# Kernel tuning notes

Measured on AMD Instinct MI355X. Metric: run time of the kernel, lower is better.

Reference implementation:

```python
import jax, jax.numpy as jnp
import numpy as np

N_HEADS = 16
EPS = 1e-12  # F.normalize default eps


def setup_inputs() -> dict:
    key = jax.random.key(0)
    ks = jax.random.split(key, 12)
    bs, qlen, dim = 2, 2048, 2048
    s = 0.02
    return {
        "input": jax.random.normal(ks[0], (bs, qlen, dim), jnp.float32),
        "mask": jax.random.randint(ks[1], (bs, qlen), 0, 2, jnp.int64),
        "Wq": jax.random.normal(ks[2], (dim, dim), jnp.float32) * s,
        "bq": jax.random.normal(ks[3], (dim,), jnp.float32) * s,
        "Wk": jax.random.normal(ks[4], (dim, dim), jnp.float32) * s,
        "bk": jax.random.normal(ks[5], (dim,), jnp.float32) * s,
        "Wv": jax.random.normal(ks[6], (dim, dim), jnp.float32) * s,
        "bv": jax.random.normal(ks[7], (dim,), jnp.float32) * s,
        "Wo": jax.random.normal(ks[8], (dim, dim), jnp.float32) * s,
        "bo": jax.random.normal(ks[9], (dim,), jnp.float32) * s,
        "attention_scale": jnp.asarray(1.0 / np.sqrt(dim // N_HEADS), jnp.float32),
    }


def _l2norm(x):
    n = jnp.sqrt(jnp.sum(x * x, axis=-1, keepdims=True))
    return x / jnp.maximum(n, EPS)


def reference(input, mask, Wq, bq, Wk, bk, Wv, bv, Wo, bo, attention_scale):
    bs, qlen, dim = input.shape
    dph = dim // N_HEADS

    def shape(x):  # [b, s, dim] -> [b, h, s, dph]
        return x.reshape(bs, -1, N_HEADS, dph).transpose(0, 2, 1, 3)

    q = shape(input @ Wq.T + bq)
    k = shape(input @ Wk.T + bk)
    v = shape(input @ Wv.T + bv)

    # normalized (cosine) attention with learned scale
    q = _l2norm(q) * attention_scale
    k = _l2norm(k)

    scores = jnp.einsum("bhqd,bhkd->bhqk", q, k)
    masked = (mask == 0)[:, None, None, :]  # [b,1,1,klen]
    scores = jnp.where(masked, -jnp.inf, scores)
    weights = jax.nn.softmax(scores.astype(jnp.float32), axis=-1).astype(scores.dtype)
    # dropout p=0.0 / eval mode -> identity
    context = jnp.einsum("bhqk,bhkd->bhqd", weights, v)
    context = context.transpose(0, 2, 1, 3).reshape(bs, qlen, dim)
    return context @ Wo.T + bo
```

## Files before the change

kernel.cpp:

```cpp
#include <hip/hip_runtime.h>
#include <hip/hip_bf16.h>
#include <stdint.h>


typedef __attribute__((ext_vector_type(8))) short bf16x8;
typedef __attribute__((ext_vector_type(4))) float f32x4;
typedef __attribute__((ext_vector_type(8))) unsigned short u16x8;

#define XN 8388608L
#define WN 4194304L

__device__ __forceinline__ float bf2f(unsigned short u) {
  union { unsigned int i; float f; } v; v.i = ((unsigned int)u) << 16; return v.f;
}
__device__ __forceinline__ unsigned short f2bf(float f) {
  union { float f; unsigned int i; } u; u.f = f;
  unsigned int r = u.i + 0x7FFFu + ((u.i >> 16) & 1u);
  return (unsigned short)(r >> 16);
}

__device__ __forceinline__ void gload_lds16(const void* g, void* l) {
  __builtin_amdgcn_global_load_lds((__attribute__((address_space(1))) void*)g,
                                   (__attribute__((address_space(3))) void*)l,
                                   16, 0, 0);
}

__global__ __launch_bounds__(256) void cast5_kernel(
    const float* __restrict__ x,  const float* __restrict__ w0,
    const float* __restrict__ w1, const float* __restrict__ w2,
    const float* __restrict__ w3, unsigned short* __restrict__ dst,
    const int* __restrict__ mask, float* __restrict__ biasf)
{
  const long total8 = (XN + 4 * WN) >> 3;
  const long tid0 = (long)blockIdx.x * blockDim.x + threadIdx.x;
  const long stride = (long)gridDim.x * blockDim.x;
  for (long i = tid0; i < total8; i += stride) {
    long e = i << 3;
    const float* src; long off;
    if (e < XN) { src = x; off = e; }
    else {
      long r = e - XN;
      int wi = (int)(r >> 22);
      off = r & (WN - 1);
      src = (wi == 0) ? w0 : (wi == 1) ? w1 : (wi == 2) ? w2 : w3;
    }
    const float4* p = (const float4*)(src + off);
    float4 a = p[0], b = p[1];
    u16x8 o;
    o[0] = f2bf(a.x); o[1] = f2bf(a.y); o[2] = f2bf(a.z); o[3] = f2bf(a.w);
    o[4] = f2bf(b.x); o[5] = f2bf(b.y); o[6] = f2bf(b.z); o[7] = f2bf(b.w);
    *(u16x8*)(dst + e) = o;
  }
  for (long j = tid0; j < 4096; j += stride)
    biasf[j] = (mask[j] != 0) ? 0.f : -1.0e5f;
}

template<int MODE>
__global__ __launch_bounds__(256) void gemm2(
    const unsigned short* __restrict__ A, const unsigned short* __restrict__ Bmat,
    const float* __restrict__ bias0, const float* __restrict__ bias1,
    void* __restrict__ Cout)
{
  constexpr int NWG = (MODE == 0) ? 1024 : 512;
  __shared__ unsigned short As[2][4096];
  __shared__ unsigned short Bs[2][4096];

  const int bid = blockIdx.x;
  const int id = (bid & 7) * (NWG / 8) + (bid >> 3);

  int mat, bx, by;
  if (MODE == 0)      { mat = id >> 9; int rem = id & 511; bx = rem & 15; by = rem >> 4; }
  else if (MODE == 1) { mat = 0; bx = id & 31; by = id >> 5; }
  else                { mat = 0; bx = id & 15; by = id >> 4; }

  const unsigned short* Bb = (MODE == 0) ? (Bmat + (long)mat * WN) : Bmat;
  const float* bias = (MODE == 0) ? (mat ? bias1 : bias0) : bias0;

  const int t    = threadIdx.x;
  const int lane = t & 63;
  const int w    = t >> 6;
  const int wr   = w >> 1, wc = w & 1;
  const int l15  = lane & 15;
  const int koff = (lane >> 4) * 8;
  const int lg4  = (lane >> 4) * 4;

  const unsigned short* Ag0 = A  + (long)(by * 128 + (t >> 2)) * 2048 + (t & 3) * 8;
  const unsigned short* Bg0 = Bb + (long)(bx * 128 + (t >> 2)) * 2048 + (t & 3) * 8;

  f32x4 acc[4][4];
  const f32x4 zero = {0.f, 0.f, 0.f, 0.f};
  #pragma unroll
  for (int m = 0; m < 4; m++)
    #pragma unroll
    for (int n = 0; n < 4; n++) acc[m][n] = zero;

  auto stage = [&](int buf, int kk) {
    const long ko = (long)kk * 32;
    gload_lds16(Ag0 + ko,              &As[buf][t * 8]);
    gload_lds16(Ag0 + 64 * 2048 + ko,  &As[buf][t * 8 + 2048]);
    gload_lds16(Bg0 + ko,              &Bs[buf][t * 8]);
    gload_lds16(Bg0 + 64 * 2048 + ko,  &Bs[buf][t * 8 + 2048]);
  };

  auto body = [&](int bufR, int kk, int bufW) {
    if (kk + 1 < 64) stage(bufW, kk + 1);
    bf16x8 af[4], bfr[4];
    #pragma unroll
    for (int m = 0; m < 4; m++)
      af[m] = *(const bf16x8*)&As[bufR][(wr * 64 + m * 16 + l15) * 32 + koff];
    #pragma unroll
    for (int n = 0; n < 4; n++)
      bfr[n] = *(const bf16x8*)&Bs[bufR][(wc * 64 + n * 16 + l15) * 32 + koff];
    __builtin_amdgcn_s_setprio(1);
    #pragma unroll
    for (int m = 0; m < 4; m++)
      #pragma unroll
      for (int n = 0; n < 4; n++)
        acc[m][n] = __builtin_amdgcn_mfma_f32_16x16x32_bf16(af[m], bfr[n], acc[m][n], 0, 0, 0);
    __builtin_amdgcn_s_setprio(0);
    asm volatile("s_waitcnt vmcnt(0)" ::: "memory");
    __builtin_amdgcn_s_barrier();
    __builtin_amdgcn_sched_barrier(0);
  };

  stage(0, 0);
  asm volatile("s_waitcnt vmcnt(0)" ::: "memory");
  __builtin_amdgcn_s_barrier();
  __builtin_amdgcn_sched_barrier(0);

  for (int kk = 0; kk < 64; kk += 2) {
    body(0, kk,     1);
    body(1, kk + 1, 0);
  }

  #pragma unroll
  for (int m = 0; m < 4; m++) {
    const int row = by * 128 + wr * 64 + m * 16 + lg4;
    #pragma unroll
    for (int n = 0; n < 4; n++) {
      const int col = bx * 128 + wc * 64 + n * 16 + l15;
      #pragma unroll
      for (int r = 0; r < 4; r++) {
        float v = acc[m][n][r];
        if (MODE == 0) {
          v += bias[col];
          ((unsigned short*)Cout + (long)mat * XN)[(long)(row + r) * 2048 + col] = f2bf(v);
        } else if (MODE == 1) {
          v += bias[row + r];
          ((unsigned short*)Cout)[(long)(row + r) * 2048 + (col & 2047)
                                  + (long)(col >> 11) * 4194304] = f2bf(v);
        } else {
          v += bias[col];
          ((float*)Cout)[(long)(row + r) * 2048 + col] = v;
        }
      }
    }
  }
}

__global__ __launch_bounds__(256) void norm_qk(unsigned short* __restrict__ Q,
                                               unsigned short* __restrict__ Kb,
                                               const float* __restrict__ scale_p)
{
  const int w = threadIdx.x >> 6, lane = threadIdx.x & 63;
  const long id = (long)blockIdx.x * 4 + w;
  const int isK = id >= 65536;
  const long p = isK ? id - 65536 : id;
  unsigned short* base = (isK ? Kb : Q) + (p >> 4) * 2048 + (p & 15) * 128 + lane * 2;
  unsigned int v = *(const unsigned int*)base;
  float x0 = bf2f((unsigned short)(v & 0xffffu));
  float x1 = bf2f((unsigned short)(v >> 16));
  float ss = x0 * x0 + x1 * x1;
  ss += __shfl_xor(ss, 1);  ss += __shfl_xor(ss, 2);  ss += __shfl_xor(ss, 4);
  ss += __shfl_xor(ss, 8);  ss += __shfl_xor(ss, 16); ss += __shfl_xor(ss, 32);
  float inv = rsqrtf(fmaxf(ss, 1e-24f));
  if (!isK) inv *= *scale_p;
  unsigned int o = (unsigned int)f2bf(x0 * inv) | ((unsigned int)f2bf(x1 * inv) << 16);
  *(unsigned int*)base = o;
}

__global__ __launch_bounds__(256, 2) void attn_kernel(
    const unsigned short* __restrict__ Q,
    const unsigned short* __restrict__ Kg_,
    const unsigned short* __restrict__ Vt_,
    const float* __restrict__ biasArr,
    unsigned short* __restrict__ ctx)
{
  __shared__ unsigned char KS[16384];
  __shared__ unsigned char VS[16384];
  __shared__ unsigned short Pl[4][32][72];

  const int bh = blockIdx.y, b = bh >> 4, h = bh & 15;
  const int t = threadIdx.x, w = t >> 6, lane = t & 63;
  const int l15 = lane & 15, lg = lane >> 4;
  const int xork = (l15 & 7) << 4;
  const int qrow0 = blockIdx.x * 128 + w * 32;

  bf16x8 aq[2][4];
  #pragma unroll
  for (int m = 0; m < 2; m++)
    #pragma unroll
    for (int dk = 0; dk < 4; dk++)
      aq[m][dk] = *(const bf16x8*)&Q[(long)(b * 2048 + qrow0 + m * 16 + l15) * 2048
                                     + h * 128 + dk * 32 + lg * 8];

  const char* Kgp = (const char*)(Kg_ + (long)b * 2048 * 2048 + h * 128);
  const char* Vgp = (const char*)(Vt_ + (long)bh * 128 * 2048);
  const int rK = t >> 4;
  const int rV = t >> 3;
  const char* srcK0 = Kgp + (long)rK * 4096 + (((t & 15) * 16) ^ ((rK & 7) << 4));
  const char* srcV0 = Vgp + (long)rV * 4096 + (((t & 7) * 16) ^ ((rV & 7) << 4));
  char* dstK0 = (char*)KS + t * 16;
  char* dstV0 = (char*)VS + t * 16;

  f32x4 o[2][8]; float den[2][4];
  const f32x4 zero = {0.f, 0.f, 0.f, 0.f};
  #pragma unroll
  for (int m = 0; m < 2; m++) {
    #pragma unroll
    for (int df = 0; df < 8; df++) o[m][df] = zero;
    #pragma unroll
    for (int r = 0; r < 4; r++) den[m][r] = 0.f;
  }

  const char* KSc = (const char*)KS;
  const char* VSc = (const char*)VS;
  int cK[4], cV2[2];
  #pragma unroll
  for (int dk = 0; dk < 4; dk++) cK[dk] = (dk * 64 + lg * 16) ^ xork;
  #pragma unroll
  for (int kk = 0; kk < 2; kk++) cV2[kk] = (kk * 64 + lg * 16) ^ xork;
  const int rowK = l15 * 256, rowV = l15 * 128;

  #pragma unroll
  for (int i = 0; i < 4; i++) gload_lds16(srcK0 + i * 65536,  dstK0 + i * 4096);
  #pragma unroll
  for (int i = 0; i < 4; i++) gload_lds16(srcV0 + i * 131072, dstV0 + i * 4096);

  const float* brow = biasArr + b * 2048 + l15;
  const float L2E = 1.44269504088896f;

  for (int kt = 0; kt < 32; kt++) {
    const int k0 = kt * 64;
    asm volatile("s_waitcnt vmcnt(4)" ::: "memory");
    __builtin_amdgcn_s_barrier();
    __builtin_amdgcn_sched_barrier(0);

    float bn[4];
    #pragma unroll
    for (int n = 0; n < 4; n++) bn[n] = brow[k0 + n * 16];

    f32x4 s[2][4];
    #pragma unroll
    for (int m = 0; m < 2; m++)
      #pragma unroll
      for (int n = 0; n < 4; n++) s[m][n] = zero;
    __builtin_amdgcn_s_setprio(1);
    #pragma unroll
    for (int n = 0; n < 4; n++) {
      #pragma unroll
      for (int dk = 0; dk < 4; dk++) {
        bf16x8 bk = *(const bf16x8*)(KSc + n * 4096 + rowK + cK[dk]);
        s[0][n] = __builtin_amdgcn_mfma_f32_16x16x32_bf16(aq[0][dk], bk, s[0][n], 0, 0, 0);
        s[1][n] = __builtin_amdgcn_mfma_f32_16x16x32_bf16(aq[1][dk], bk, s[1][n], 0, 0, 0);
      }
    }
    __builtin_amdgcn_s_setprio(0);

    #pragma unroll
    for (int n = 0; n < 4; n++) {
      #pragma unroll
      for (int m = 0; m < 2; m++) {
        #pragma unroll
        for (int r = 0; r < 4; r++) {
          float e = exp2f(fmaf(s[m][n][r], L2E, bn[n]));
          den[m][r] += e;
          Pl[w][m * 16 + lg * 4 + r][n * 16 + l15] = f2bf(e);
        }
      }
    }

    asm volatile("s_waitcnt vmcnt(0)" ::: "memory");
    __builtin_amdgcn_s_barrier();
    __builtin_amdgcn_sched_barrier(0);
    if (kt < 31) {
      const long kof = (long)(kt + 1) * 262144;
      #pragma unroll
      for (int i = 0; i < 4; i++) gload_lds16(srcK0 + kof + i * 65536, dstK0 + i * 4096);
    }

    #pragma unroll
    for (int kk = 0; kk < 2; kk++) {
      bf16x8 ap0 = *(const bf16x8*)&Pl[w][l15][kk * 32 + lg * 8];
      bf16x8 ap1 = *(const bf16x8*)&Pl[w][16 + l15][kk * 32 + lg * 8];
      bf16x8 bv[8];
      #pragma unroll
      for (int df = 0; df < 8; df++)
        bv[df] = *(const bf16x8*)(VSc + df * 2048 + rowV + cV2[kk]);
      __builtin_amdgcn_s_setprio(1);
      #pragma unroll
      for (int df = 0; df < 8; df++) {
        o[0][df] = __builtin_amdgcn_mfma_f32_16x16x32_bf16(ap0, bv[df], o[0][df], 0, 0, 0);
        o[1][df] = __builtin_amdgcn_mfma_f32_16x16x32_bf16(ap1, bv[df], o[1][df], 0, 0, 0);
      }
      __builtin_amdgcn_s_setprio(0);
    }

    __builtin_amdgcn_s_barrier();
    __builtin_amdgcn_sched_barrier(0);
    if (kt < 31) {
      const long vof = (long)(kt + 1) * 128;
      #pragma unroll
      for (int i = 0; i < 4; i++) gload_lds16(srcV0 + vof + i * 131072, dstV0 + i * 4096);
    }
  }

  #pragma unroll
  for (int m = 0; m < 2; m++)
    #pragma unroll
    for (int r = 0; r < 4; r++) {
      float d = den[m][r];
      d += __shfl_xor(d, 1); d += __shfl_xor(d, 2);
      d += __shfl_xor(d, 4); d += __shfl_xor(d, 8);
      den[m][r] = 1.0f / d;
    }
  #pragma unroll
  for (int m = 0; m < 2; m++) {
    const long row = b * 2048 + qrow0 + m * 16 + lg * 4;
    #pragma unroll
    for (int df = 0; df < 8; df++) {
      const int col = h * 128 + df * 16 + l15;
      #pragma unroll
      for (int r = 0; r < 4; r++)
        ctx[(row + r) * 2048 + col] = f2bf(o[m][df][r] * den[m][r]);
    }
  }
}

extern "C" void kernel_launch(void* const* d_in, const int* in_sizes, int n_in,
                              void* d_out, int out_size, void* d_ws, size_t ws_size,
                              hipStream_t stream) {
  const float* x    = (const float*)d_in[0];
  const int*   mask = (const int*)d_in[1];
  const float* Wq   = (const float*)d_in[2];
  const float* bq   = (const float*)d_in[3];
  const float* Wk   = (const float*)d_in[4];
  const float* bk   = (const float*)d_in[5];
  const float* Wv   = (const float*)d_in[6];
  const float* bv   = (const float*)d_in[7];
  const float* Wo   = (const float*)d_in[8];
  const float* bo   = (const float*)d_in[9];
  const float* asc  = (const float*)d_in[10];
  float* out = (float*)d_out;

  unsigned short* w   = (unsigned short*)d_ws;
  unsigned short* Xb  = w;
  unsigned short* Wqb = Xb  + XN;
  unsigned short* Wvb = Wqb + 2 * WN;
  unsigned short* Wob = Wvb + WN;
  unsigned short* Qb  = Wob + WN;
  unsigned short* Kbf = Qb  + XN;
  unsigned short* Vt  = Kbf + XN;
  float*          Bias = (float*)(Vt + XN);
  unsigned short* Ctx = Xb;

  cast5_kernel<<<2048, 256, 0, stream>>>(x, Wq, Wk, Wv, Wo, Xb, mask, Bias);

  gemm2<0><<<1024, 256, 0, stream>>>(Xb, Wqb, bq, bk, Qb);
  gemm2<1><<<512,  256, 0, stream>>>(Wvb, Xb, bv, bv, Vt);

  norm_qk<<<32768, 256, 0, stream>>>(Qb, Kbf, asc);

  attn_kernel<<<dim3(16, 32), 256, 0, stream>>>(Qb, Kbf, Vt, Bias, Ctx);

  gemm2<2><<<512, 256, 0, stream>>>(Ctx, Wob, bo, bo, out);
}
```

Before: 459.5 us.

## Replace 128x128 GEMM with 256x256-tile 8-wave kernel using swizzled LDS

The projection GEMMs move from 128x128 tiles with 4 waves and a K-step of 32 to 256x256 tiles with 8 waves, a K-step of 128 split into two halves, and a 128 KB double-buffered LDS region with an XOR swizzle. Each wave now holds an 8x4 grid of accumulators, and loads for the next tile are interleaved with MFMA groups under finer vmcnt waits. The aim is to raise arithmetic intensity, cut global traffic per FLOP and avoid LDS bank conflicts. In exchange it launches far fewer workgroups (128-256 on a GPU with many CUs), which risks under-filling the device, and it raises register and LDS pressure.

```diff
diff --git a/kernel.cpp b/kernel.cpp
--- a/kernel.cpp
+++ b/kernel.cpp
@@ -56,92 +56,155 @@
 }
 
 template<int MODE>
-__global__ __launch_bounds__(256) void gemm2(
+__global__ __launch_bounds__(512, 2) void gemm8(
     const unsigned short* __restrict__ A, const unsigned short* __restrict__ Bmat,
     const float* __restrict__ bias0, const float* __restrict__ bias1,
     void* __restrict__ Cout)
 {
-  constexpr int NWG = (MODE == 0) ? 1024 : 512;
-  __shared__ unsigned short As[2][4096];
-  __shared__ unsigned short Bs[2][4096];
+  constexpr int NWG = (MODE == 0) ? 256 : 128;
+  constexpr int NT = 32;
+  __shared__ char LDSb[131072];
 
   const int bid = blockIdx.x;
   const int id = (bid & 7) * (NWG / 8) + (bid >> 3);
 
   int mat, bx, by;
-  if (MODE == 0)      { mat = id >> 9; int rem = id & 511; bx = rem & 15; by = rem >> 4; }
-  else if (MODE == 1) { mat = 0; bx = id & 31; by = id >> 5; }
-  else                { mat = 0; bx = id & 15; by = id >> 4; }
-
-  const unsigned short* Bb = (MODE == 0) ? (Bmat + (long)mat * WN) : Bmat;
-  const float* bias = (MODE == 0) ? (mat ? bias1 : bias0) : bias0;
-
-  const int t    = threadIdx.x;
-  const int lane = t & 63;
-  const int w    = t >> 6;
-  const int wr   = w >> 1, wc = w & 1;
-  const int l15  = lane & 15;
-  const int koff = (lane >> 4) * 8;
-  const int lg4  = (lane >> 4) * 4;
-
-  const unsigned short* Ag0 = A  + (long)(by * 128 + (t >> 2)) * 2048 + (t & 3) * 8;
-  const unsigned short* Bg0 = Bb + (long)(bx * 128 + (t >> 2)) * 2048 + (t & 3) * 8;
-
-  f32x4 acc[4][4];
+  if (MODE == 0)      { mat = id >> 7; int rem = id & 127; bx = rem & 7;  by = rem >> 3; }
+  else if (MODE == 1) { mat = 0;       bx = id & 15; by = id >> 4; }
+  else                { mat = 0;       bx = id & 7;  by = id >> 3; }
+
+  const unsigned short* Ab = A + (long)(by * 256) * 2048;
+  const unsigned short* Bb = ((MODE == 0) ? (Bmat + (long)mat * WN) : Bmat)
+                             + (long)(bx * 256) * 2048;
+  const float* bias = (MODE == 0 && mat) ? bias1 : bias0;
+
+  const int t = threadIdx.x;
+  const int wid = t >> 6, lane = t & 63;
+  const int wr = wid >> 2, wc = wid & 3;
+  const int l15 = lane & 15, lg = lane >> 4;
+
+  const int p0 = t, p1 = t + 512;
+  const int sw0 = ((p0 & 3) ^ ((p0 >> 3) & 3)) << 4;
+  const int sw1 = ((p1 & 3) ^ ((p1 >> 3) & 3)) << 4;
+  const char* srcA0 = (const char*)Ab + (long)(p0 >> 2) * 4096 + sw0;
+  const char* srcA1 = (const char*)Ab + (long)(p1 >> 2) * 4096 + sw1;
+  const char* srcB0 = (const char*)Bb + (long)(p0 >> 2) * 4096 + sw0;
+  const char* srcB1 = (const char*)Bb + (long)(p1 >> 2) * 4096 + sw1;
+  char* dA0 = LDSb + p0 * 16;
+  char* dA1 = LDSb + p1 * 16;
+  char* dB0 = LDSb + 16384 + p0 * 16;
+  char* dB1 = LDSb + 16384 + p1 * 16;
+
+  auto stage = [&](int buf, int kh, int tile) {
+    const long go = (long)kh * 64 + (long)tile * 128;
+    const int lo = buf * 65536 + kh * 32768;
+    gload_lds16(srcA0 + go, dA0 + lo);
+    gload_lds16(srcA1 + go, dA1 + lo);
+    gload_lds16(srcB0 + go, dB0 + lo);
+    gload_lds16(srcB1 + go, dB1 + lo);
+  };
+
+  const int koffL = ((lg ^ ((l15 >> 1) & 3)) << 4) + l15 * 64;
+  const int aBase0 = (wr * 128) * 64;
+  const int bBase  = 16384 + (wc * 64) * 64;
+
+  f32x4 acc[8][4];
   const f32x4 zero = {0.f, 0.f, 0.f, 0.f};
   #pragma unroll
-  for (int m = 0; m < 4; m++)
+  for (int m = 0; m < 8; m++)
     #pragma unroll
     for (int n = 0; n < 4; n++) acc[m][n] = zero;
 
-  auto stage = [&](int buf, int kk) {
-    const long ko = (long)kk * 32;
-    gload_lds16(Ag0 + ko,              &As[buf][t * 8]);
-    gload_lds16(Ag0 + 64 * 2048 + ko,  &As[buf][t * 8 + 2048]);
-    gload_lds16(Bg0 + ko,              &Bs[buf][t * 8]);
-    gload_lds16(Bg0 + 64 * 2048 + ko,  &Bs[buf][t * 8 + 2048]);
-  };
-
-  auto body = [&](int bufR, int kk, int bufW) {
-    if (kk + 1 < 64) stage(bufW, kk + 1);
-    bf16x8 af[4], bfr[4];
-    #pragma unroll
-    for (int m = 0; m < 4; m++)
-      af[m] = *(const bf16x8*)&As[bufR][(wr * 64 + m * 16 + l15) * 32 + koff];
-    #pragma unroll
-    for (int n = 0; n < 4; n++)
-      bfr[n] = *(const bf16x8*)&Bs[bufR][(wc * 64 + n * 16 + l15) * 32 + koff];
-    __builtin_amdgcn_s_setprio(1);
-    #pragma unroll
-    for (int m = 0; m < 4; m++)
-      #pragma unroll
-      for (int n = 0; n < 4; n++)
-        acc[m][n] = __builtin_amdgcn_mfma_f32_16x16x32_bf16(af[m], bfr[n], acc[m][n], 0, 0, 0);
-    __builtin_amdgcn_s_setprio(0);
-    asm volatile("s_waitcnt vmcnt(0)" ::: "memory");
-    __builtin_amdgcn_s_barrier();
-    __builtin_amdgcn_sched_barrier(0);
-  };
-
-  stage(0, 0);
-  asm volatile("s_waitcnt vmcnt(0)" ::: "memory");
+  stage(0, 0, 0);
+  stage(0, 1, 0);
+  asm volatile("s_waitcnt vmcnt(4)" ::: "memory");
   __builtin_amdgcn_s_barrier();
   __builtin_amdgcn_sched_barrier(0);
 
-  for (int kk = 0; kk < 64; kk += 2) {
-    body(0, kk,     1);
-    body(1, kk + 1, 0);
-  }
-
-  #pragma unroll
-  for (int m = 0; m < 4; m++) {
-    const int row = by * 128 + wr * 64 + m * 16 + lg4;
+  int cur = 0;
+  bf16x8 a0, a1, a2, a3, b0, b1, b2, b3;
+
+  #define RD_A(buf, kh, mh) do {                                             \
+    const char* p_ = LDSb + (buf) * 65536 + (kh) * 32768                     \
+                     + aBase0 + (mh) * 4096 + koffL;                         \
+    a0 = *(const bf16x8*)(p_);        a1 = *(const bf16x8*)(p_ + 1024);      \
+    a2 = *(const bf16x8*)(p_ + 2048); a3 = *(const bf16x8*)(p_ + 3072); } while (0)
+  #define RD_B(buf, kh) do {                                                 \
+    const char* p_ = LDSb + (buf) * 65536 + (kh) * 32768 + bBase + koffL;    \
+    b0 = *(const bf16x8*)(p_);        b1 = *(const bf16x8*)(p_ + 1024);      \
+    b2 = *(const bf16x8*)(p_ + 2048); b3 = *(const bf16x8*)(p_ + 3072); } while (0)
+  #define MFMA16(mo) do {                                                    \
+    __builtin_amdgcn_s_setprio(1);                                           \
+    acc[mo+0][0] = __builtin_amdgcn_mfma_f32_16x16x32_bf16(a0, b0, acc[mo+0][0],0,0,0); \
+    acc[mo+0][1] = __builtin_amdgcn_mfma_f32_16x16x32_bf16(a0, b1, acc[mo+0][1],0,0,0); \
+    acc[mo+0][2] = __builtin_amdgcn_mfma_f32_16x16x32_bf16(a0, b2, acc[mo+0][2],0,0,0); \
+    acc[mo+0][3] = __builtin_amdgcn_mfma_f32_16x16x32_bf16(a0, b3, acc[mo+0][3],0,0,0); \
+    acc[mo+1][0] = __builtin_amdgcn_mfma_f32_16x16x32_bf16(a1, b0, acc[mo+1][0],0,0,0); \
+    acc[mo+1][1] = __builtin_amdgcn_mfma_f32_16x16x32_bf16(a1, b1, acc[mo+1][1],0,0,0); \
+    acc[mo+1][2] = __builtin_amdgcn_mfma_f32_16x16x32_bf16(a1, b2, acc[mo+1][2],0,0,0); \
+    acc[mo+1][3] = __builtin_amdgcn_mfma_f32_16x16x32_bf16(a1, b3, acc[mo+1][3],0,0,0); \
+    acc[mo+2][0] = __builtin_amdgcn_mfma_f32_16x16x32_bf16(a2, b0, acc[mo+2][0],0,0,0); \
+    acc[mo+2][1] = __builtin_amdgcn_mfma_f32_16x16x32_bf16(a2, b1, acc[mo+2][1],0,0,0); \
+    acc[mo+2][2] = __builtin_amdgcn_mfma_f32_16x16x32_bf16(a2, b2, acc[mo+2][2],0,0,0); \
+    acc[mo+2][3] = __builtin_amdgcn_mfma_f32_16x16x32_bf16(a2, b3, acc[mo+2][3],0,0,0); \
+    acc[mo+3][0] = __builtin_amdgcn_mfma_f32_16x16x32_bf16(a3, b0, acc[mo+3][0],0,0,0); \
+    acc[mo+3][1] = __builtin_amdgcn_mfma_f32_16x16x32_bf16(a3, b1, acc[mo+3][1],0,0,0); \
+    acc[mo+3][2] = __builtin_amdgcn_mfma_f32_16x16x32_bf16(a3, b2, acc[mo+3][2],0,0,0); \
+    acc[mo+3][3] = __builtin_amdgcn_mfma_f32_16x16x32_bf16(a3, b3, acc[mo+3][3],0,0,0); \
+    __builtin_amdgcn_s_setprio(0); } while (0)
+
+  for (int tt = 0; tt < NT - 1; tt++) {
+    const int nxt = cur ^ 1;
+    stage(nxt, 0, tt + 1);
+    RD_B(cur, 0); RD_A(cur, 0, 0);
+    MFMA16(0);
+    __builtin_amdgcn_s_barrier();
+    __builtin_amdgcn_sched_barrier(0);
+    RD_A(cur, 0, 1);
+    MFMA16(4);
+    asm volatile("s_waitcnt vmcnt(4)" ::: "memory");
+    __builtin_amdgcn_s_barrier();
+    __builtin_amdgcn_sched_barrier(0);
+    stage(nxt, 1, tt + 1);
+    RD_B(cur, 1); RD_A(cur, 1, 0);
+    MFMA16(0);
+    __builtin_amdgcn_s_barrier();
+    __builtin_amdgcn_sched_barrier(0);
+    RD_A(cur, 1, 1);
+    MFMA16(4);
+    asm volatile("s_waitcnt vmcnt(4)" ::: "memory");
+    __builtin_amdgcn_s_barrier();
+    __builtin_amdgcn_sched_barrier(0);
+    cur = nxt;
+  }
+  {
+    RD_B(cur, 0); RD_A(cur, 0, 0);
+    MFMA16(0);
+    __builtin_amdgcn_s_barrier();
+    __builtin_amdgcn_sched_barrier(0);
+    RD_A(cur, 0, 1);
+    MFMA16(4);
+    asm volatile("s_waitcnt vmcnt(0)" ::: "memory");
+    __builtin_amdgcn_s_barrier();
+    __builtin_amdgcn_sched_barrier(0);
+    RD_B(cur, 1); RD_A(cur, 1, 0);
+    MFMA16(0);
+    RD_A(cur, 1, 1);
+    MFMA16(4);
+  }
+  #undef RD_A
+  #undef RD_B
+  #undef MFMA16
+
+  #pragma unroll
+  for (int am = 0; am < 8; am++) {
+    const int row = by * 256 + wr * 128 + am * 16 + lg * 4;
     #pragma unroll
     for (int n = 0; n < 4; n++) {
-      const int col = bx * 128 + wc * 64 + n * 16 + l15;
+      const int col = bx * 256 + wc * 64 + n * 16 + l15;
       #pragma unroll
       for (int r = 0; r < 4; r++) {
-        float v = acc[m][n][r];
+        float v = acc[am][n][r];
         if (MODE == 0) {
           v += bias[col];
           ((unsigned short*)Cout + (long)mat * XN)[(long)(row + r) * 2048 + col] = f2bf(v);
@@ -366,12 +429,12 @@
 
   cast5_kernel<<<2048, 256, 0, stream>>>(x, Wq, Wk, Wv, Wo, Xb, mask, Bias);
 
-  gemm2<0><<<1024, 256, 0, stream>>>(Xb, Wqb, bq, bk, Qb);
-  gemm2<1><<<512,  256, 0, stream>>>(Wvb, Xb, bv, bv, Vt);
+  gemm8<0><<<256, 512, 0, stream>>>(Xb, Wqb, bq, bk, Qb);
+  gemm8<1><<<128, 512, 0, stream>>>(Wvb, Xb, bv, bv, Vt);
 
   norm_qk<<<32768, 256, 0, stream>>>(Qb, Kbf, asc);
 
   attn_kernel<<<dim3(16, 32), 256, 0, stream>>>(Qb, Kbf, Vt, Bias, Ctx);
 
-  gemm2<2><<<512, 256, 0, stream>>>(Ctx, Wob, bo, bo, out);
-}
+  gemm8<2><<<128, 512, 0, stream>>>(Ctx, Wob, bo, bo, out);
+}
```

New measurement: 450.4 us. 2.0% less time.

## Replace 128x128 GEMM with 8-wave 256-row tiles, swizzled LDS and 64-K stages

Applied to the files above, without the earlier changes.

Rewrites the projection GEMMs to use 512-thread workgroups with larger output tiles (256x256 for QK, 256x128 otherwise) and 128-wide K steps split into two halves. LDS is XOR-swizzled to avoid bank conflicts, and loads are double-buffered with finer-grained waitcnt and barrier interleaving. The aim is more data reuse per global load and better MFMA utilisation. The trade-off is large LDS use (up to 128KB), fewer workgroups (256), and more register pressure.

```diff
diff --git a/kernel.cpp b/kernel.cpp
--- a/kernel.cpp
+++ b/kernel.cpp
@@ -56,92 +56,183 @@
 }
 
 template<int MODE>
-__global__ __launch_bounds__(256) void gemm2(
+__global__ __launch_bounds__(512, 2) void gemm8(
     const unsigned short* __restrict__ A, const unsigned short* __restrict__ Bmat,
     const float* __restrict__ bias0, const float* __restrict__ bias1,
     void* __restrict__ Cout)
 {
-  constexpr int NWG = (MODE == 0) ? 1024 : 512;
-  __shared__ unsigned short As[2][4096];
-  __shared__ unsigned short Bs[2][4096];
+  constexpr int NWG = 256;
+  constexpr int NT  = 32;
+  constexpr int KHS = (MODE == 0) ? 32768 : 24576;
+  constexpr int BUFS = 2 * KHS;
+  __shared__ char LDSb[(MODE == 0) ? 131072 : 98304];
 
   const int bid = blockIdx.x;
   const int id = (bid & 7) * (NWG / 8) + (bid >> 3);
 
   int mat, bx, by;
-  if (MODE == 0)      { mat = id >> 9; int rem = id & 511; bx = rem & 15; by = rem >> 4; }
+  if (MODE == 0)      { mat = id >> 7; int rem = id & 127; bx = rem & 7;  by = rem >> 3; }
   else if (MODE == 1) { mat = 0; bx = id & 31; by = id >> 5; }
   else                { mat = 0; bx = id & 15; by = id >> 4; }
 
-  const unsigned short* Bb = (MODE == 0) ? (Bmat + (long)mat * WN) : Bmat;
-  const float* bias = (MODE == 0) ? (mat ? bias1 : bias0) : bias0;
-
-  const int t    = threadIdx.x;
-  const int lane = t & 63;
-  const int w    = t >> 6;
-  const int wr   = w >> 1, wc = w & 1;
-  const int l15  = lane & 15;
-  const int koff = (lane >> 4) * 8;
-  const int lg4  = (lane >> 4) * 4;
-
-  const unsigned short* Ag0 = A  + (long)(by * 128 + (t >> 2)) * 2048 + (t & 3) * 8;
-  const unsigned short* Bg0 = Bb + (long)(bx * 128 + (t >> 2)) * 2048 + (t & 3) * 8;
-
-  f32x4 acc[4][4];
+  constexpr int BN = (MODE == 0) ? 256 : 128;
+  const unsigned short* Ab = A + (long)(by * 256) * 2048;
+  const unsigned short* Bb = ((MODE == 0) ? (Bmat + (long)mat * WN) : Bmat)
+                             + (long)(bx * BN) * 2048;
+  const float* bias = (MODE == 0 && mat) ? bias1 : bias0;
+
+  const int t = threadIdx.x;
+  const int wid = t >> 6, lane = t & 63;
+  const int wr = (MODE == 0) ? (wid >> 2) : (wid >> 1);
+  const int wc = (MODE == 0) ? (wid & 3)  : (wid & 1);
+  const int l15 = lane & 15, lg = lane >> 4;
+
+  const int pA0 = t, pA1 = t + 512;
+  auto sw = [](int p) { return (((p & 3) ^ ((p >> 3) & 3)) << 4); };
+  const char* srcA0 = (const char*)Ab + (long)(pA0 >> 2) * 4096 + sw(pA0);
+  const char* srcA1 = (const char*)Ab + (long)(pA1 >> 2) * 4096 + sw(pA1);
+  const char* srcB0 = (const char*)Bb + (long)(pA0 >> 2) * 4096 + sw(pA0);
+  const char* srcB1 = (const char*)Bb + (long)(pA1 >> 2) * 4096 + sw(pA1);
+
+  auto stage = [&](int buf, int kh, int tile) {
+    const long go = (long)tile * 128 + kh * 64;
+    char* base = LDSb + buf * BUFS + kh * KHS;
+    gload_lds16(srcA0 + go, base + pA0 * 16);
+    gload_lds16(srcA1 + go, base + pA1 * 16);
+    if (MODE == 0) {
+      gload_lds16(srcB0 + go, base + 16384 + pA0 * 16);
+      gload_lds16(srcB1 + go, base + 16384 + pA1 * 16);
+    } else {
+      gload_lds16(srcB0 + go, base + 16384 + t * 16);
+    }
+  };
+
+  const int slot16 = ((lg ^ ((l15 >> 1) & 3)) << 4);
+  const int aRowOff = ((MODE == 0) ? (wr * 128) : (wr * 64)) * 64 + l15 * 64 + slot16;
+  const int bColOff = 16384 + (wc * 64) * 64 + l15 * 64 + slot16;
+
+  constexpr int AM = (MODE == 0) ? 8 : 4;
+  f32x4 acc[AM][4];
   const f32x4 zero = {0.f, 0.f, 0.f, 0.f};
   #pragma unroll
-  for (int m = 0; m < 4; m++)
+  for (int m = 0; m < AM; m++)
     #pragma unroll
     for (int n = 0; n < 4; n++) acc[m][n] = zero;
 
-  auto stage = [&](int buf, int kk) {
-    const long ko = (long)kk * 32;
-    gload_lds16(Ag0 + ko,              &As[buf][t * 8]);
-    gload_lds16(Ag0 + 64 * 2048 + ko,  &As[buf][t * 8 + 2048]);
-    gload_lds16(Bg0 + ko,              &Bs[buf][t * 8]);
-    gload_lds16(Bg0 + 64 * 2048 + ko,  &Bs[buf][t * 8 + 2048]);
-  };
-
-  auto body = [&](int bufR, int kk, int bufW) {
-    if (kk + 1 < 64) stage(bufW, kk + 1);
-    bf16x8 af[4], bfr[4];
-    #pragma unroll
-    for (int m = 0; m < 4; m++)
-      af[m] = *(const bf16x8*)&As[bufR][(wr * 64 + m * 16 + l15) * 32 + koff];
-    #pragma unroll
-    for (int n = 0; n < 4; n++)
-      bfr[n] = *(const bf16x8*)&Bs[bufR][(wc * 64 + n * 16 + l15) * 32 + koff];
-    __builtin_amdgcn_s_setprio(1);
-    #pragma unroll
-    for (int m = 0; m < 4; m++)
-      #pragma unroll
-      for (int n = 0; n < 4; n++)
-        acc[m][n] = __builtin_amdgcn_mfma_f32_16x16x32_bf16(af[m], bfr[n], acc[m][n], 0, 0, 0);
-    __builtin_amdgcn_s_setprio(0);
-    asm volatile("s_waitcnt vmcnt(0)" ::: "memory");
-    __builtin_amdgcn_s_barrier();
-    __builtin_amdgcn_sched_barrier(0);
-  };
-
-  stage(0, 0);
-  asm volatile("s_waitcnt vmcnt(0)" ::: "memory");
-  __builtin_amdgcn_s_barrier();
-  __builtin_amdgcn_sched_barrier(0);
-
-  for (int kk = 0; kk < 64; kk += 2) {
-    body(0, kk,     1);
-    body(1, kk + 1, 0);
-  }
-
-  #pragma unroll
-  for (int m = 0; m < 4; m++) {
-    const int row = by * 128 + wr * 64 + m * 16 + lg4;
+  bf16x8 a_[4], b_[4];
+
+  #define RD_A(buf, kh, mh) do {                                              \
+    const char* p_ = LDSb + (buf) * BUFS + (kh) * KHS + aRowOff + (mh) * 4096;\
+    a_[0] = *(const bf16x8*)(p_);        a_[1] = *(const bf16x8*)(p_ + 1024); \
+    a_[2] = *(const bf16x8*)(p_ + 2048); a_[3] = *(const bf16x8*)(p_ + 3072); } while (0)
+  #define RD_B(buf, kh) do {                                                  \
+    const char* p_ = LDSb + (buf) * BUFS + (kh) * KHS + bColOff;              \
+    b_[0] = *(const bf16x8*)(p_);        b_[1] = *(const bf16x8*)(p_ + 1024); \
+    b_[2] = *(const bf16x8*)(p_ + 2048); b_[3] = *(const bf16x8*)(p_ + 3072); } while (0)
+  #define CL(amB) do {                                                        \
+    __builtin_amdgcn_s_setprio(1);                                            \
+    _Pragma("unroll")                                                         \
+    for (int i_ = 0; i_ < 4; i_++)                                            \
+      _Pragma("unroll")                                                       \
+      for (int n_ = 0; n_ < 4; n_++)                                          \
+        acc[(amB) + i_][n_] = __builtin_amdgcn_mfma_f32_16x16x32_bf16(        \
+            a_[i_], b_[n_], acc[(amB) + i_][n_], 0, 0, 0);                    \
+    __builtin_amdgcn_s_setprio(0); } while (0)
+  #define SB0   __builtin_amdgcn_sched_barrier(0)
+  #define BAR   __builtin_amdgcn_s_barrier()
+  #define LGKM0 asm volatile("s_waitcnt lgkmcnt(0)" ::: "memory")
+  #define VMW(n) asm volatile("s_waitcnt vmcnt(" #n ")" ::: "memory")
+
+  stage(0, 0, 0);
+  stage(0, 1, 0);
+  if (MODE == 0) VMW(4); else VMW(3);
+  BAR; SB0;
+
+  int cur = 0;
+  for (int tt = 0; tt < NT - 1; tt++) {
+    const int nxt = cur ^ 1;
+    if (MODE == 0) {
+      RD_A(cur, 0, 0); RD_B(cur, 0);
+      stage(nxt, 0, tt + 1);
+      SB0; BAR; LGKM0; SB0;
+      CL(0);
+      BAR;
+      RD_A(cur, 0, 1);
+      SB0; BAR; LGKM0; SB0;
+      CL(4);
+      VMW(4);
+      BAR;
+      RD_A(cur, 1, 0); RD_B(cur, 1);
+      stage(nxt, 1, tt + 1);
+      SB0; BAR; LGKM0; SB0;
+      CL(0);
+      BAR;
+      RD_A(cur, 1, 1);
+      SB0; BAR; LGKM0; SB0;
+      CL(4);
+      VMW(4);
+      BAR;
+    } else {
+      RD_A(cur, 0, 0); RD_B(cur, 0);
+      stage(nxt, 0, tt + 1);
+      SB0; BAR; LGKM0; SB0;
+      CL(0);
+      VMW(3);
+      BAR;
+      RD_A(cur, 1, 0); RD_B(cur, 1);
+      stage(nxt, 1, tt + 1);
+      SB0; BAR; LGKM0; SB0;
+      CL(0);
+      VMW(3);
+      BAR;
+    }
+    cur = nxt;
+  }
+  if (MODE == 0) {
+    RD_A(cur, 0, 0); RD_B(cur, 0);
+    SB0; BAR; LGKM0; SB0;
+    CL(0);
+    BAR;
+    RD_A(cur, 0, 1);
+    SB0; BAR; LGKM0; SB0;
+    CL(4);
+    VMW(0);
+    BAR;
+    RD_A(cur, 1, 0); RD_B(cur, 1);
+    SB0; BAR; LGKM0; SB0;
+    CL(0);
+    BAR;
+    RD_A(cur, 1, 1);
+    SB0; LGKM0; SB0;
+    CL(4);
+  } else {
+    RD_A(cur, 0, 0); RD_B(cur, 0);
+    SB0; BAR; LGKM0; SB0;
+    CL(0);
+    VMW(0);
+    BAR;
+    RD_A(cur, 1, 0); RD_B(cur, 1);
+    SB0; LGKM0; SB0;
+    CL(0);
+  }
+  #undef RD_A
+  #undef RD_B
+  #undef CL
+  #undef SB0
+  #undef BAR
+  #undef LGKM0
+  #undef VMW
+
+  const int rowW = (MODE == 0) ? (wr * 128) : (wr * 64);
+  #pragma unroll
+  for (int am = 0; am < AM; am++) {
+    const int row = by * 256 + rowW + am * 16 + lg * 4;
     #pragma unroll
     for (int n = 0; n < 4; n++) {
-      const int col = bx * 128 + wc * 64 + n * 16 + l15;
+      const int col = bx * BN + wc * 64 + n * 16 + l15;
       #pragma unroll
       for (int r = 0; r < 4; r++) {
-        float v = acc[m][n][r];
+        float v = acc[am][n][r];
         if (MODE == 0) {
           v += bias[col];
           ((unsigned short*)Cout + (long)mat * XN)[(long)(row + r) * 2048 + col] = f2bf(v);
@@ -366,12 +457,12 @@
 
   cast5_kernel<<<2048, 256, 0, stream>>>(x, Wq, Wk, Wv, Wo, Xb, mask, Bias);
 
-  gemm2<0><<<1024, 256, 0, stream>>>(Xb, Wqb, bq, bk, Qb);
-  gemm2<1><<<512,  256, 0, stream>>>(Wvb, Xb, bv, bv, Vt);
+  gemm8<0><<<256, 512, 0, stream>>>(Xb, Wqb, bq, bk, Qb);
+  gemm8<1><<<256, 512, 0, stream>>>(Wvb, Xb, bv, bv, Vt);
 
   norm_qk<<<32768, 256, 0, stream>>>(Qb, Kbf, asc);
 
   attn_kernel<<<dim3(16, 32), 256, 0, stream>>>(Qb, Kbf, Vt, Bias, Ctx);
 
-  gemm2<2><<<512, 256, 0, stream>>>(Ctx, Wob, bo, bo, out);
-}
+  gemm8<2><<<256, 512, 0, stream>>>(Ctx, Wob, bo, bo, out);
+}
```

Result: faster. 416.7 us (-9.3%).
